# Kernel optimization log

Hardware: AMD Instinct MI355X
Metric: run time of the kernel (lower is better)

Reference implementation:

```python
import jax, jax.numpy as jnp
import numpy as np

N_ATOMS = 50000
IN_DIM = 128
HID = 256
N_ELEM = 4
N_IMG = 500
NNZ = 2_000_000
ELEMENTS = jnp.array([1, 6, 8, 29], dtype=jnp.int64)


def setup_inputs() -> dict:
    key = jax.random.key(0)
    ks = jax.random.split(key, 14)
    fingerprints = jax.random.normal(ks[0], (N_ATOMS, IN_DIM), dtype=jnp.float32)
    # atomic numbers drawn from the supported element set
    elem_idx = jax.random.randint(ks[1], (N_ATOMS,), 0, N_ELEM)
    atomic_numbers = ELEMENTS[elem_idx]
    image_idx = jnp.sort(jax.random.randint(ks[2], (N_ATOMS,), 0, N_IMG))
    # sparse fprimes (COO): [N_ATOMS*IN_DIM, 3*N_ATOMS]
    fprime_rows = jax.random.randint(ks[3], (NNZ,), 0, N_ATOMS * IN_DIM)
    fprime_cols = jax.random.randint(ks[4], (NNZ,), 0, 3 * N_ATOMS)
    fprime_vals = jax.random.normal(ks[5], (NNZ,), dtype=jnp.float32) * 0.1
    # per-element MLP params, stacked over the element axis (torch Linear-style init)
    s0, s1 = 1.0 / np.sqrt(IN_DIM), 1.0 / np.sqrt(HID)
    W0 = jax.random.uniform(ks[6], (N_ELEM, IN_DIM, HID), jnp.float32, -s0, s0)
    b0 = jax.random.uniform(ks[7], (N_ELEM, HID), jnp.float32, -s0, s0)
    W1 = jax.random.uniform(ks[8], (N_ELEM, HID, HID), jnp.float32, -s1, s1)
    b1 = jax.random.uniform(ks[9], (N_ELEM, HID), jnp.float32, -s1, s1)
    W2 = jax.random.uniform(ks[10], (N_ELEM, HID, 1), jnp.float32, -s1, s1)
    b2 = jax.random.uniform(ks[11], (N_ELEM, 1), jnp.float32, -s1, s1)
    return {"fingerprints": fingerprints, "atomic_numbers": atomic_numbers,
            "image_idx": image_idx, "fprime_rows": fprime_rows,
            "fprime_cols": fprime_cols, "fprime_vals": fprime_vals,
            "W0": W0, "b0": b0, "W1": W1, "b1": b1, "W2": W2, "b2": b2}


def _per_atom_energy(fp, atomic_numbers, W0, b0, W1, b1, W2, b2):
    # Run every element-specific MLP over ALL atoms (as the torch module does),
    # then mask by the one-hot element membership and sum over elements.
    h = jnp.tanh(jnp.einsum('nd,edh->enh', fp, W0) + b0[:, None, :])   # [E,N,H]
    h = jnp.tanh(jnp.einsum('enh,ehk->enk', h, W1) + b1[:, None, :])   # [E,N,H]
    out = jnp.einsum('enh,eho->eno', h, W2) + b2[:, None, :]           # [E,N,1]
    mask = (atomic_numbers[None, :] == ELEMENTS[:, None]).astype(fp.dtype)  # [E,N]
    return jnp.sum(mask * out[..., 0], axis=0)                          # [N]


def reference(fingerprints, atomic_numbers, image_idx, fprime_rows,
              fprime_cols, fprime_vals, W0, b0, W1, b1, W2, b2):
    o = _per_atom_energy(fingerprints, atomic_numbers, W0, b0, W1, b1, W2, b2)
    energy = jax.ops.segment_sum(o, image_idx, num_segments=N_IMG)  # [N_IMG]
    # dE/dfp for forces (sum over images == sum over atoms of o)
    g = jax.grad(lambda fp: jnp.sum(
        _per_atom_energy(fp, atomic_numbers, W0, b0, W1, b1, W2, b2)))(fingerprints)
    g_flat = g.reshape(-1)  # [N*D]
    # forces = -fprimes^T @ g_flat, fprimes in COO form
    forces = -jax.ops.segment_sum(fprime_vals * g_flat[fprime_rows],
                                  fprime_cols, num_segments=3 * N_ATOMS)
    return energy, forces.reshape(N_ATOMS, 3)
```

## Files before the change

### kernel.cpp

```cpp
#include <hip/hip_runtime.h>
#include <math.h>

#define N_ATOMS 50000
#define IN_DIM 128
#define HID 256
#define N_ELEM 4
#define N_IMG 500
#define NNZ 2000000

#define CBINS 293
#define CW 512
#define BCAP 8192
#define OCAP 4096
#define PCH 8192
#define NBP ((NNZ + PCH - 1) / PCH)

typedef __attribute__((ext_vector_type(8))) short bf16x8;
typedef __attribute__((ext_vector_type(4))) float f32x4;
typedef __attribute__((ext_vector_type(4))) int   i32x4;
typedef __attribute__((ext_vector_type(4))) float fv4;

__device__ __forceinline__ int elem_of(int z) {
    return (z == 1) ? 0 : (z == 6) ? 1 : (z == 8) ? 2 : 3;
}

__device__ __forceinline__ unsigned short f2bf(float f) {
    unsigned u = __float_as_uint(f);
    u += 0x7fffu + ((u >> 16) & 1u);
    return (unsigned short)(u >> 16);
}
__device__ __forceinline__ float bf2f(unsigned short u) {
    return __uint_as_float(((unsigned)u) << 16);
}
__device__ __forceinline__ float tanh_fast(float x) {
    float e = __expf(2.f * x);
    return (e - 1.f) / (e + 1.f);
}

__global__ __launch_bounds__(256) void bucket_kernel(
    const int* __restrict__ Z, int* __restrict__ counts, int* __restrict__ lists,
    float* __restrict__ F) {
    for (int idx = blockIdx.x * blockDim.x + threadIdx.x; idx < 3 * N_ATOMS;
         idx += gridDim.x * blockDim.x) F[idx] = 0.f;
    __shared__ int lcnt[N_ELEM], lbase[N_ELEM];
    const int i = blockIdx.x * blockDim.x + threadIdx.x;
    if (threadIdx.x < N_ELEM) lcnt[threadIdx.x] = 0;
    __syncthreads();
    int e = -1, pos = 0;
    if (i < N_ATOMS) {
        e = elem_of(Z[i]);
        pos = atomicAdd(&lcnt[e], 1);
    }
    __syncthreads();
    if (threadIdx.x < N_ELEM)
        lbase[threadIdx.x] = atomicAdd(&counts[threadIdx.x], lcnt[threadIdx.x]);
    __syncthreads();
    if (i < N_ATOMS) lists[e * N_ATOMS + lbase[e] + pos] = i;
}

__global__ __launch_bounds__(256) void prep_weights(
    const float* __restrict__ W0, const float* __restrict__ W1,
    unsigned short* __restrict__ W0s1,
    unsigned short* __restrict__ W1s2,
    unsigned short* __restrict__ W1s3,
    unsigned short* __restrict__ W0s4,
    int* __restrict__ counts, int* __restrict__ gcur, int* __restrict__ ocur) {
    if (blockIdx.x == 0) {
        if (threadIdx.x < N_ELEM) counts[threadIdx.x] = 0;
        for (int i = threadIdx.x; i < CBINS; i += 256) gcur[i] = 0;
        if (threadIdx.x == 0) ocur[0] = 0;
    }
    int t = blockIdx.x * 256 + threadIdx.x;
    if (t >= N_ELEM * HID * HID) return;
    int e = t >> 16;
    int rem = t & 65535;
    int k = rem >> 8, n = rem & 255;
    unsigned short w1 = f2bf(W1[t]);
    {
        int lane = (((k >> 3) & 3) << 4) | (n & 15);
        W1s2[(e << 16) + ((((n >> 4) * 8 + (k >> 5)) * 64 + lane) << 3) + (k & 7)] = w1;
    }
    {
        int lane = (((n >> 3) & 3) << 4) | (k & 15);
        W1s3[(e << 16) + ((((k >> 4) * 8 + (n >> 5)) * 64 + lane) << 3) + (n & 7)] = w1;
    }
    if (k < IN_DIM) {
        unsigned short w0 = f2bf(W0[e * (IN_DIM * HID) + rem]);
        {
            int lane = (((k >> 3) & 3) << 4) | (n & 15);
            W0s1[e * (IN_DIM * HID) + ((((n >> 4) * 4 + (k >> 5)) * 64 + lane) << 3) + (k & 7)] = w0;
        }
        {
            int lane = (((n >> 3) & 3) << 4) | (k & 15);
            W0s4[e * (IN_DIM * HID) + ((((k >> 4) * 8 + (n >> 5)) * 64 + lane) << 3) + (n & 7)] = w0;
        }
    }
}

__global__ __launch_bounds__(256) void bin_producer(
    const int* __restrict__ rows, const int* __restrict__ cols,
    const float* __restrict__ vals,
    int* __restrict__ rowsB, int* __restrict__ colsB, float* __restrict__ valsB,
    int* __restrict__ gcur,
    int* __restrict__ ovfR, int* __restrict__ ovfC, float* __restrict__ ovfV,
    int* __restrict__ ocur) {

    __shared__ int   Lr[PCH];
    __shared__ int   Lc[PCH];
    __shared__ float Lv[PCH];
    __shared__ int   hist[CBINS], pref[CBINS], curs[CBINS], gbase[CBINS];

    const int tid = threadIdx.x;
    const int base = blockIdx.x * PCH;

    for (int i = tid; i < CBINS; i += 256) hist[i] = 0;
    __syncthreads();

    i32x4 r[8], c[8];
    fv4   v[8];
    int nvalid[8];
#pragma unroll
    for (int j = 0; j < 8; ++j) {
        const int i0 = base + tid * 4 + 1024 * j;
        int nv = NNZ - i0;
        nvalid[j] = nv > 4 ? 4 : (nv < 0 ? 0 : nv);
        if (nvalid[j] == 4) {
            r[j] = __builtin_nontemporal_load((const i32x4*)(rows + i0));
            c[j] = __builtin_nontemporal_load((const i32x4*)(cols + i0));
            v[j] = __builtin_nontemporal_load((const fv4*)(vals + i0));
        } else {
            for (int e2 = 0; e2 < nvalid[j]; ++e2) {
                r[j][e2] = rows[i0 + e2]; c[j][e2] = cols[i0 + e2];
                v[j][e2] = vals[i0 + e2];
            }
        }
#pragma unroll
        for (int e2 = 0; e2 < 4; ++e2)
            if (e2 < nvalid[j]) atomicAdd(&hist[c[j][e2] >> 9], 1);
    }
    __syncthreads();

    if (tid == 0) {
        int s = 0;
        for (int b = 0; b < CBINS; ++b) { pref[b] = s; s += hist[b]; }
    }
    __syncthreads();
    for (int b = tid; b < CBINS; b += 256) {
        gbase[b] = atomicAdd(&gcur[b], hist[b]);
        curs[b] = pref[b];
    }
    __syncthreads();

#pragma unroll
    for (int j = 0; j < 8; ++j)
#pragma unroll
        for (int e2 = 0; e2 < 4; ++e2)
            if (e2 < nvalid[j]) {
                int b = c[j][e2] >> 9;
                int p = atomicAdd(&curs[b], 1);
                Lr[p] = r[j][e2]; Lc[p] = c[j][e2]; Lv[p] = v[j][e2];
            }
    __syncthreads();

    const int total = (base + PCH <= NNZ) ? PCH : (NNZ - base);
#pragma unroll
    for (int j = 0; j < 32; ++j) {
        const int p = tid + 256 * j;
        if (p >= total) break;
        const int col = Lc[p];
        const int b = col >> 9;
        const int g = gbase[b] + (p - pref[b]);
        if (g < BCAP) {
            rowsB[b * BCAP + g] = Lr[p];
            colsB[b * BCAP + g] = col;
            valsB[b * BCAP + g] = Lv[p];
        } else {
            int od = atomicAdd(ocur, 1);
            if (od < OCAP) { ovfR[od] = Lr[p]; ovfC[od] = col; ovfV[od] = Lv[p]; }
        }
    }
}

#define TILES_PER_E 512
__global__ __launch_bounds__(256, 4) void fused_mlp(
    const float* __restrict__ fp,
    const unsigned short* __restrict__ W0s1,
    const unsigned short* __restrict__ W1s2,
    const unsigned short* __restrict__ W1s3,
    const unsigned short* __restrict__ W0s4,
    const float* __restrict__ b0, const float* __restrict__ b1,
    const float* __restrict__ W2, const float* __restrict__ b2,
    float* __restrict__ o_atom,
    unsigned short* __restrict__ Gb,
    const int* __restrict__ counts, const int* __restrict__ lists) {

    const int bid = blockIdx.x;
    const int xcd = bid & 7;
    const int e = xcd & 3;
    const int tile = (bid >> 3) * 2 + (xcd >> 2);
    const int cnt = counts[e];
    const int m0 = tile * 32;
    if (m0 >= cnt) return;
    const int* list = lists + e * N_ATOMS;

    __shared__ short tH[8 * 32 * 34];
    __shared__ short tD[8 * 32 * 34];
    __shared__ float red[4][32];

    const int tid = threadIdx.x;
    const int lane = tid & 63;
    const int wv = tid >> 6;
    const int lr = lane & 15;
    const int lq = lane >> 4;

    const unsigned short* B1 = W0s1 + (size_t)e * HID * IN_DIM;
    const unsigned short* B2 = W1s2 + (size_t)e * HID * HID;
    const unsigned short* B3 = W1s3 + (size_t)e * HID * HID;
    const unsigned short* B4 = W0s4 + (size_t)e * IN_DIM * HID;

    const float* arow[2];
    bool aok[2];
#pragma unroll
    for (int mt = 0; mt < 2; ++mt) {
        int m = m0 + mt * 16 + lr;
        aok[mt] = (m < cnt);
        arow[mt] = aok[mt] ? (fp + (size_t)list[m] * IN_DIM) : fp;
    }

    f32x4 acc[2][4];
#define ZERO_ACC()                                                        \
    _Pragma("unroll") for (int mt = 0; mt < 2; ++mt)                      \
        _Pragma("unroll") for (int nt = 0; nt < 4; ++nt)                  \
            _Pragma("unroll") for (int j = 0; j < 4; ++j) acc[mt][nt][j] = 0.f;

    ZERO_ACC();
    {
        float4 a0[2][2], a1[2][2];
        bf16x8 bb[2][4];
#pragma unroll
        for (int mt = 0; mt < 2; ++mt) if (aok[mt]) {
            a0[0][mt] = *(const float4*)(arow[mt] + lq * 8);
            a1[0][mt] = *(const float4*)(arow[mt] + lq * 8 + 4);
        }
#pragma unroll
        for (int nt = 0; nt < 4; ++nt)
            bb[0][nt] = *(const bf16x8*)(B1 +
                ((size_t)(((wv * 4 + nt) * 4 + 0) * 64 + lane) << 3));
#pragma unroll
        for (int ki = 0; ki < 4; ++ki) {
            const int cur = ki & 1, nx = cur ^ 1;
            if (ki < 3) {
                const int k0n = (ki + 1) * 32;
#pragma unroll
                for (int mt = 0; mt < 2; ++mt) if (aok[mt]) {
                    a0[nx][mt] = *(const float4*)(arow[mt] + k0n + lq * 8);
                    a1[nx][mt] = *(const float4*)(arow[mt] + k0n + lq * 8 + 4);
                }
#pragma unroll
                for (int nt = 0; nt < 4; ++nt)
                    bb[nx][nt] = *(const bf16x8*)(B1 +
                        ((size_t)(((wv * 4 + nt) * 4 + ki + 1) * 64 + lane) << 3));
            }
            bf16x8 af[2];
#pragma unroll
            for (int mt = 0; mt < 2; ++mt) {
                bf16x8 vv;
#pragma unroll
                for (int j = 0; j < 8; ++j) vv[j] = 0;
                if (aok[mt]) {
                    vv[0] = (short)f2bf(a0[cur][mt].x); vv[1] = (short)f2bf(a0[cur][mt].y);
                    vv[2] = (short)f2bf(a0[cur][mt].z); vv[3] = (short)f2bf(a0[cur][mt].w);
                    vv[4] = (short)f2bf(a1[cur][mt].x); vv[5] = (short)f2bf(a1[cur][mt].y);
                    vv[6] = (short)f2bf(a1[cur][mt].z); vv[7] = (short)f2bf(a1[cur][mt].w);
                }
                af[mt] = vv;
            }
#pragma unroll
            for (int mt = 0; mt < 2; ++mt)
#pragma unroll
                for (int nt = 0; nt < 4; ++nt)
                    acc[mt][nt] = __builtin_amdgcn_mfma_f32_16x16x32_bf16(
                        af[mt], bb[cur][nt], acc[mt][nt], 0, 0, 0);
        }
    }

    bf16x8 b2r[3][4];
#pragma unroll
    for (int p = 0; p < 3; ++p)
#pragma unroll
        for (int nt = 0; nt < 4; ++nt)
            b2r[p][nt] = *(const bf16x8*)(B2 +
                ((size_t)(((wv * 4 + nt) * 8 + p) * 64 + lane) << 3));

    {
        float bv[4];
#pragma unroll
        for (int nt = 0; nt < 4; ++nt)
            bv[nt] = b0[e * HID + wv * 64 + nt * 16 + lr];
#pragma unroll
        for (int mt = 0; mt < 2; ++mt)
#pragma unroll
            for (int rr = 0; rr < 4; ++rr) {
                const int row = mt * 16 + lq * 4 + rr;
#pragma unroll
                for (int nt = 0; nt < 4; ++nt) {
                    const int n = wv * 64 + nt * 16 + lr;
                    float t = tanh_fast(acc[mt][nt][rr] + bv[nt]);
                    tH[(n >> 5) * 1088 + row * 34 + (n & 31)] = (short)f2bf(t);
                }
            }
    }
    __syncthreads();

    ZERO_ACC();
#pragma unroll
    for (int ki = 0; ki < 8; ++ki) {
        bf16x8 af[2];
#pragma unroll
        for (int mt = 0; mt < 2; ++mt)
            af[mt] = *(const bf16x8*)&tH[ki * 1088 + (mt * 16 + lr) * 34 + lq * 8];
#pragma unroll
        for (int mt = 0; mt < 2; ++mt)
#pragma unroll
            for (int nt = 0; nt < 4; ++nt)
                acc[mt][nt] = __builtin_amdgcn_mfma_f32_16x16x32_bf16(
                    af[mt], b2r[ki % 3][nt], acc[mt][nt], 0, 0, 0);
        if (ki < 5) {
#pragma unroll
            for (int nt = 0; nt < 4; ++nt)
                b2r[ki % 3][nt] = *(const bf16x8*)(B2 +
                    ((size_t)(((wv * 4 + nt) * 8 + ki + 3) * 64 + lane) << 3));
        }
    }

    bf16x8 b3r[3][4];
#pragma unroll
    for (int p = 0; p < 3; ++p)
#pragma unroll
        for (int nt = 0; nt < 4; ++nt)
            b3r[p][nt] = *(const bf16x8*)(B3 +
                ((size_t)(((wv * 4 + nt) * 8 + p) * 64 + lane) << 3));

    {
        float bv[4], w2v[4];
#pragma unroll
        for (int nt = 0; nt < 4; ++nt) {
            bv[nt]  = b1[e * HID + wv * 64 + nt * 16 + lr];
            w2v[nt] = W2[e * HID + wv * 64 + nt * 16 + lr];
        }
#pragma unroll
        for (int mt = 0; mt < 2; ++mt)
#pragma unroll
            for (int rr = 0; rr < 4; ++rr) {
                const int row = mt * 16 + lq * 4 + rr;
                float osum = 0.f;
#pragma unroll
                for (int nt = 0; nt < 4; ++nt) {
                    const int n = wv * 64 + nt * 16 + lr;
                    float t = tanh_fast(acc[mt][nt][rr] + bv[nt]);
                    osum += t * w2v[nt];
                    tD[(n >> 5) * 1088 + row * 34 + (n & 31)] =
                        (short)f2bf(w2v[nt] * (1.f - t * t));
                }
                osum += __shfl_xor(osum, 1, 64);
                osum += __shfl_xor(osum, 2, 64);
                osum += __shfl_xor(osum, 4, 64);
                osum += __shfl_xor(osum, 8, 64);
                if (lr == 0) red[wv][row] = osum;
            }
    }
    __syncthreads();
    if (tid < 32) {
        int m = m0 + tid;
        if (m < cnt)
            o_atom[list[m]] = red[0][tid] + red[1][tid] + red[2][tid] +
                              red[3][tid] + b2[e];
    }

    ZERO_ACC();
#pragma unroll
    for (int ki = 0; ki < 8; ++ki) {
        bf16x8 af[2];
#pragma unroll
        for (int mt = 0; mt < 2; ++mt)
            af[mt] = *(const bf16x8*)&tD[ki * 1088 + (mt * 16 + lr) * 34 + lq * 8];
#pragma unroll
        for (int mt = 0; mt < 2; ++mt)
#pragma unroll
            for (int nt = 0; nt < 4; ++nt)
                acc[mt][nt] = __builtin_amdgcn_mfma_f32_16x16x32_bf16(
                    af[mt], b3r[ki % 3][nt], acc[mt][nt], 0, 0, 0);
        if (ki < 5) {
#pragma unroll
            for (int nt = 0; nt < 4; ++nt)
                b3r[ki % 3][nt] = *(const bf16x8*)(B3 +
                    ((size_t)(((wv * 4 + nt) * 8 + ki + 3) * 64 + lane) << 3));
        }
    }

    bf16x8 b4r[3][2];
#pragma unroll
    for (int p = 0; p < 3; ++p)
#pragma unroll
        for (int nt = 0; nt < 2; ++nt)
            b4r[p][nt] = *(const bf16x8*)(B4 +
                ((size_t)(((wv * 2 + nt) * 8 + p) * 64 + lane) << 3));

#pragma unroll
    for (int mt = 0; mt < 2; ++mt)
#pragma unroll
        for (int rr = 0; rr < 4; ++rr) {
            const int row = mt * 16 + lq * 4 + rr;
#pragma unroll
            for (int nt = 0; nt < 4; ++nt) {
                const int n = wv * 64 + nt * 16 + lr;
                const int a = (n >> 5) * 1088 + row * 34 + (n & 31);
                float h = bf2f((unsigned short)tH[a]);
                tH[a] = (short)f2bf(acc[mt][nt][rr] * (1.f - h * h));
            }
        }
    __syncthreads();

    {
        f32x4 a4[2][2];
#pragma unroll
        for (int mt = 0; mt < 2; ++mt)
#pragma unroll
            for (int nt = 0; nt < 2; ++nt)
#pragma unroll
                for (int j = 0; j < 4; ++j) a4[mt][nt][j] = 0.f;
#pragma unroll
        for (int ki = 0; ki < 8; ++ki) {
            bf16x8 af[2];
#pragma unroll
            for (int mt = 0; mt < 2; ++mt)
                af[mt] = *(const bf16x8*)&tH[ki * 1088 + (mt * 16 + lr) * 34 + lq * 8];
#pragma unroll
            for (int mt = 0; mt < 2; ++mt)
#pragma unroll
                for (int nt = 0; nt < 2; ++nt)
                    a4[mt][nt] = __builtin_amdgcn_mfma_f32_16x16x32_bf16(
                        af[mt], b4r[ki % 3][nt], a4[mt][nt], 0, 0, 0);
            if (ki < 5) {
#pragma unroll
                for (int nt = 0; nt < 2; ++nt)
                    b4r[ki % 3][nt] = *(const bf16x8*)(B4 +
                        ((size_t)(((wv * 2 + nt) * 8 + ki + 3) * 64 + lane) << 3));
            }
        }
#pragma unroll
        for (int mt = 0; mt < 2; ++mt)
#pragma unroll
            for (int rr = 0; rr < 4; ++rr) {
                const int row = mt * 16 + lq * 4 + rr;
#pragma unroll
                for (int nt = 0; nt < 2; ++nt) {
                    const int n = wv * 32 + nt * 16 + lr;
                    tD[(n >> 5) * 1088 + row * 34 + (n & 31)] =
                        (short)f2bf(a4[mt][nt][rr]);
                }
            }
    }
    __syncthreads();
#pragma unroll
    for (int t = 0; t < 2; ++t) {
        const int c = tid + 256 * t;
        const int row = c >> 4;
        const int pos = (c & 15) * 8;
        const int m = m0 + row;
        if (m < cnt) {
            bf16x8 v = *(const bf16x8*)&tD[(pos >> 5) * 1088 + row * 34 + (pos & 31)];
            *(bf16x8*)(Gb + (size_t)list[m] * IN_DIM + pos) = v;
        }
    }
#undef ZERO_ACC
}

__global__ __launch_bounds__(1024) void forces_consumer(
    const int* __restrict__ rowsB, const int* __restrict__ colsB,
    const float* __restrict__ valsB, const int* __restrict__ gcur,
    const unsigned short* __restrict__ g, float* __restrict__ F,
    const float* __restrict__ o_atom, const int* __restrict__ img,
    float* __restrict__ energy,
    const int* __restrict__ ovfR, const int* __restrict__ ovfC,
    const float* __restrict__ ovfV, const int* __restrict__ ocur) {

    const int blk = blockIdx.x;
    __shared__ float win[CW];

    if (blk < CBINS) {
        for (int i = threadIdx.x; i < CW; i += 1024) win[i] = 0.f;
        __syncthreads();
        const int w0 = blk << 9;
        int cnt = gcur[blk]; if (cnt > BCAP) cnt = BCAP;
        const size_t o = (size_t)blk * BCAP;
        for (int idx0 = (int)threadIdx.x * 4; idx0 < cnt; idx0 += 4096) {
            if (idx0 + 4 <= cnt) {
                i32x4 r = *(const i32x4*)(rowsB + o + idx0);
                i32x4 c = *(const i32x4*)(colsB + o + idx0);
                fv4   v = *(const fv4*)(valsB + o + idx0);
                float g0 = bf2f(g[r[0]]), g1 = bf2f(g[r[1]]);
                float g2 = bf2f(g[r[2]]), g3 = bf2f(g[r[3]]);
                atomicAdd(&win[c[0] - w0], -v[0] * g0);
                atomicAdd(&win[c[1] - w0], -v[1] * g1);
                atomicAdd(&win[c[2] - w0], -v[2] * g2);
                atomicAdd(&win[c[3] - w0], -v[3] * g3);
            } else {
                for (int e2 = idx0; e2 < cnt; ++e2)
                    atomicAdd(&win[colsB[o + e2] - w0],
                              -valsB[o + e2] * bf2f(g[rowsB[o + e2]]));
            }
        }
        int ocnt = ocur[0]; if (ocnt > OCAP) ocnt = OCAP;
        for (int k2 = threadIdx.x; k2 < ocnt; k2 += 1024) {
            int c = ovfC[k2];
            if (c >= w0 && c < w0 + CW)
                atomicAdd(&win[c - w0], -ovfV[k2] * bf2f(g[ovfR[k2]]));
        }
        __syncthreads();
        for (int i = threadIdx.x; i < CW; i += 1024) {
            int c = w0 + i;
            if (c < 3 * N_ATOMS) F[c] = win[i];
        }
    }

    if (blk < N_IMG) {
        const int bb = blk;
        int lo, hi;
        {
            int l = 0, r = N_ATOMS;
            while (l < r) { int m = (l + r) >> 1; if (img[m] < bb) l = m + 1; else r = m; }
            lo = l;
        }
        {
            int l = lo, r = N_ATOMS;
            while (l < r) { int m = (l + r) >> 1; if (img[m] < bb + 1) l = m + 1; else r = m; }
            hi = l;
        }
        float s = 0.f;
        for (int i2 = lo + (int)threadIdx.x; i2 < hi; i2 += 1024) s += o_atom[i2];
#pragma unroll
        for (int off = 32; off > 0; off >>= 1) s += __shfl_down(s, off, 64);
        __shared__ float red[16];
        if ((threadIdx.x & 63) == 0) red[threadIdx.x >> 6] = s;
        __syncthreads();
        if (threadIdx.x == 0) {
            float t = 0.f;
#pragma unroll
            for (int w = 0; w < 16; ++w) t += red[w];
            energy[bb] = t;
        }
    }
}

extern "C" void kernel_launch(void* const* d_in, const int* in_sizes, int n_in,
                              void* d_out, int out_size, void* d_ws, size_t ws_size,
                              hipStream_t stream) {
    const float* fp    = (const float*)d_in[0];
    const int*   Z     = (const int*)d_in[1];
    const int*   img   = (const int*)d_in[2];
    const int*   frows = (const int*)d_in[3];
    const int*   fcols = (const int*)d_in[4];
    const float* fvals = (const float*)d_in[5];
    const float* W0    = (const float*)d_in[6];
    const float* b0    = (const float*)d_in[7];
    const float* W1    = (const float*)d_in[8];
    const float* b1    = (const float*)d_in[9];
    const float* W2    = (const float*)d_in[10];
    const float* b2    = (const float*)d_in[11];

    float* out    = (float*)d_out;
    float* energy = out;
    float* F      = out + N_IMG;

    char* ws = (char*)d_ws;
    int*   counts = (int*)ws;
    int*   lists  = (int*)(ws + 1024);
    char*  base   = ws + (1 << 20);
    unsigned short* Gb   = (unsigned short*)(base);
    float* o_atom        = (float*)(base + 13000000);
    unsigned short* W0s1 = (unsigned short*)(base + 14000000);
    unsigned short* W0s4 = W0s1 + N_ELEM * IN_DIM * HID;
    unsigned short* W1s2 = W0s4 + N_ELEM * IN_DIM * HID;
    unsigned short* W1s3 = W1s2 + N_ELEM * HID * HID;
    int*   gcur  = (int*)(base + 18000000);
    int*   ocur  = (int*)(base + 18002048);
    int*   rowsB = (int*)(base + 19000000);
    int*   colsB = (int*)(base + 29000000);
    float* valsB = (float*)(base + 39000000);
    int*   ovfR  = (int*)(base + 49000000);
    int*   ovfC  = (int*)(base + 49050000);
    float* ovfV  = (float*)(base + 49100000);

    prep_weights<<<(N_ELEM * HID * HID + 255) / 256, 256, 0, stream>>>(
        W0, W1, W0s1, W1s2, W1s3, W0s4, counts, gcur, ocur);
    bucket_kernel<<<(N_ATOMS + 255) / 256, 256, 0, stream>>>(Z, counts, lists, F);
    bin_producer<<<NBP, 256, 0, stream>>>(
        frows, fcols, fvals, rowsB, colsB, valsB, gcur, ovfR, ovfC, ovfV, ocur);

    fused_mlp<<<8 * (TILES_PER_E / 2), 256, 0, stream>>>(
        fp, W0s1, W1s2, W1s3, W0s4, b0, b1, W2, b2, o_atom, Gb, counts, lists);

    forces_consumer<<<N_IMG, 1024, 0, stream>>>(
        rowsB, colsB, valsB, gcur, Gb, F, o_atom, img, energy,
        ovfR, ovfC, ovfV, ocur);
}
```

Measured before the change: 231.7 us.

## Merge atom bucketing into bin producer and repad MLP LDS tiles

```diff
diff --git a/kernel.cpp b/kernel.cpp
--- a/kernel.cpp
+++ b/kernel.cpp
@@ -14,6 +14,7 @@
 #define OCAP 4096
 #define PCH 8192
 #define NBP ((NNZ + PCH - 1) / PCH)
+#define BKB ((N_ATOMS + 255) / 256)
 
 typedef __attribute__((ext_vector_type(8))) short bf16x8;
 typedef __attribute__((ext_vector_type(4))) float f32x4;
@@ -35,27 +36,6 @@
 __device__ __forceinline__ float tanh_fast(float x) {
     float e = __expf(2.f * x);
     return (e - 1.f) / (e + 1.f);
-}
-
-__global__ __launch_bounds__(256) void bucket_kernel(
-    const int* __restrict__ Z, int* __restrict__ counts, int* __restrict__ lists,
-    float* __restrict__ F) {
-    for (int idx = blockIdx.x * blockDim.x + threadIdx.x; idx < 3 * N_ATOMS;
-         idx += gridDim.x * blockDim.x) F[idx] = 0.f;
-    __shared__ int lcnt[N_ELEM], lbase[N_ELEM];
-    const int i = blockIdx.x * blockDim.x + threadIdx.x;
-    if (threadIdx.x < N_ELEM) lcnt[threadIdx.x] = 0;
-    __syncthreads();
-    int e = -1, pos = 0;
-    if (i < N_ATOMS) {
-        e = elem_of(Z[i]);
-        pos = atomicAdd(&lcnt[e], 1);
-    }
-    __syncthreads();
-    if (threadIdx.x < N_ELEM)
-        lbase[threadIdx.x] = atomicAdd(&counts[threadIdx.x], lcnt[threadIdx.x]);
-    __syncthreads();
-    if (i < N_ATOMS) lists[e * N_ATOMS + lbase[e] + pos] = i;
 }
 
 __global__ __launch_bounds__(256) void prep_weights(
@@ -97,7 +77,9 @@
     }
 }
 
-__global__ __launch_bounds__(256) void bin_producer(
+__global__ __launch_bounds__(256) void bucket_and_bin(
+    const int* __restrict__ Z, int* __restrict__ counts, int* __restrict__ lists,
+    float* __restrict__ F,
     const int* __restrict__ rows, const int* __restrict__ cols,
     const float* __restrict__ vals,
     int* __restrict__ rowsB, int* __restrict__ colsB, float* __restrict__ valsB,
@@ -111,6 +93,29 @@
     __shared__ int   hist[CBINS], pref[CBINS], curs[CBINS], gbase[CBINS];
 
     const int tid = threadIdx.x;
+
+    if (blockIdx.x >= NBP) {
+        int* lcnt = hist;
+        int* lbase = pref;
+        const int bb = blockIdx.x - NBP;
+        for (int idx = bb * 256 + tid; idx < 3 * N_ATOMS; idx += BKB * 256)
+            F[idx] = 0.f;
+        const int i = bb * 256 + tid;
+        if (tid < N_ELEM) lcnt[tid] = 0;
+        __syncthreads();
+        int e = -1, pos = 0;
+        if (i < N_ATOMS) {
+            e = elem_of(Z[i]);
+            pos = atomicAdd(&lcnt[e], 1);
+        }
+        __syncthreads();
+        if (tid < N_ELEM)
+            lbase[tid] = atomicAdd(&counts[tid], lcnt[tid]);
+        __syncthreads();
+        if (i < N_ATOMS) lists[e * N_ATOMS + lbase[e] + pos] = i;
+        return;
+    }
+
     const int base = blockIdx.x * PCH;
 
     for (int i = tid; i < CBINS; i += 256) hist[i] = 0;
@@ -182,7 +187,8 @@
 }
 
 #define TILES_PER_E 512
-__global__ __launch_bounds__(256, 4) void fused_mlp(
+#define CH 1280
+__global__ __launch_bounds__(256, 3) void fused_mlp(
     const float* __restrict__ fp,
     const unsigned short* __restrict__ W0s1,
     const unsigned short* __restrict__ W1s2,
@@ -203,8 +209,8 @@
     if (m0 >= cnt) return;
     const int* list = lists + e * N_ATOMS;
 
-    __shared__ short tH[8 * 32 * 34];
-    __shared__ short tD[8 * 32 * 34];
+    __shared__ short tH[8 * CH];
+    __shared__ short tD[8 * CH];
     __shared__ float red[4][32];
 
     const int tid = threadIdx.x;
@@ -306,7 +312,7 @@
                 for (int nt = 0; nt < 4; ++nt) {
                     const int n = wv * 64 + nt * 16 + lr;
                     float t = tanh_fast(acc[mt][nt][rr] + bv[nt]);
-                    tH[(n >> 5) * 1088 + row * 34 + (n & 31)] = (short)f2bf(t);
+                    tH[(n >> 5) * CH + row * 40 + (n & 31)] = (short)f2bf(t);
                 }
             }
     }
@@ -318,7 +324,7 @@
         bf16x8 af[2];
 #pragma unroll
         for (int mt = 0; mt < 2; ++mt)
-            af[mt] = *(const bf16x8*)&tH[ki * 1088 + (mt * 16 + lr) * 34 + lq * 8];
+            af[mt] = *(const bf16x8*)&tH[ki * CH + (mt * 16 + lr) * 40 + lq * 8];
 #pragma unroll
         for (int mt = 0; mt < 2; ++mt)
 #pragma unroll
@@ -359,7 +365,7 @@
                     const int n = wv * 64 + nt * 16 + lr;
                     float t = tanh_fast(acc[mt][nt][rr] + bv[nt]);
                     osum += t * w2v[nt];
-                    tD[(n >> 5) * 1088 + row * 34 + (n & 31)] =
+                    tD[(n >> 5) * CH + row * 40 + (n & 31)] =
                         (short)f2bf(w2v[nt] * (1.f - t * t));
                 }
                 osum += __shfl_xor(osum, 1, 64);
@@ -383,7 +389,7 @@
         bf16x8 af[2];
 #pragma unroll
         for (int mt = 0; mt < 2; ++mt)
-            af[mt] = *(const bf16x8*)&tD[ki * 1088 + (mt * 16 + lr) * 34 + lq * 8];
+            af[mt] = *(const bf16x8*)&tD[ki * CH + (mt * 16 + lr) * 40 + lq * 8];
 #pragma unroll
         for (int mt = 0; mt < 2; ++mt)
 #pragma unroll
@@ -414,7 +420,7 @@
 #pragma unroll
             for (int nt = 0; nt < 4; ++nt) {
                 const int n = wv * 64 + nt * 16 + lr;
-                const int a = (n >> 5) * 1088 + row * 34 + (n & 31);
+                const int a = (n >> 5) * CH + row * 40 + (n & 31);
                 float h = bf2f((unsigned short)tH[a]);
                 tH[a] = (short)f2bf(acc[mt][nt][rr] * (1.f - h * h));
             }
@@ -434,7 +440,7 @@
             bf16x8 af[2];
 #pragma unroll
             for (int mt = 0; mt < 2; ++mt)
-                af[mt] = *(const bf16x8*)&tH[ki * 1088 + (mt * 16 + lr) * 34 + lq * 8];
+                af[mt] = *(const bf16x8*)&tH[ki * CH + (mt * 16 + lr) * 40 + lq * 8];
 #pragma unroll
             for (int mt = 0; mt < 2; ++mt)
 #pragma unroll
@@ -456,7 +462,7 @@
 #pragma unroll
                 for (int nt = 0; nt < 2; ++nt) {
                     const int n = wv * 32 + nt * 16 + lr;
-                    tD[(n >> 5) * 1088 + row * 34 + (n & 31)] =
+                    tD[(n >> 5) * CH + row * 40 + (n & 31)] =
                         (short)f2bf(a4[mt][nt][rr]);
                 }
             }
@@ -469,7 +475,7 @@
         const int pos = (c & 15) * 8;
         const int m = m0 + row;
         if (m < cnt) {
-            bf16x8 v = *(const bf16x8*)&tD[(pos >> 5) * 1088 + row * 34 + (pos & 31)];
+            bf16x8 v = *(const bf16x8*)&tD[(pos >> 5) * CH + row * 40 + (pos & 31)];
             *(bf16x8*)(Gb + (size_t)list[m] * IN_DIM + pos) = v;
         }
     }
@@ -594,9 +600,10 @@
 
     prep_weights<<<(N_ELEM * HID * HID + 255) / 256, 256, 0, stream>>>(
         W0, W1, W0s1, W1s2, W1s3, W0s4, counts, gcur, ocur);
-    bucket_kernel<<<(N_ATOMS + 255) / 256, 256, 0, stream>>>(Z, counts, lists, F);
-    bin_producer<<<NBP, 256, 0, stream>>>(
-        frows, fcols, fvals, rowsB, colsB, valsB, gcur, ovfR, ovfC, ovfV, ocur);
+
+    bucket_and_bin<<<NBP + BKB, 256, 0, stream>>>(
+        Z, counts, lists, F, frows, fcols, fvals,
+        rowsB, colsB, valsB, gcur, ovfR, ovfC, ovfV, ocur);
 
     fused_mlp<<<8 * (TILES_PER_E / 2), 256, 0, stream>>>(
         fp, W0s1, W1s2, W1s3, W0s4, b0, b1, W2, b2, o_atom, Gb, counts, lists);
```

New measurement: 218.6 us. -5.7%, faster.
